# Kernel tuning notes

Hardware: AMD Instinct MI355X
Metric: run time of the kernel (lower is better)

## Reference

```python
import jax, jax.numpy as jnp
import numpy as np

N = 50000   # nodes
E = 500000  # edges
S = 64      # 0e channels in node feats
V = 32      # 1o channels in node feats
R = 32      # radial/scalar edge features
MLPW = 128
AVG = 10.0  # avg_num_neighbors
SQ3 = np.float32(np.sqrt(3.0))
SQ2 = np.float32(np.sqrt(2.0))


def setup_inputs() -> dict:
    key = jax.random.key(0)
    ks = jax.random.split(key, 10)
    node_scalars = jax.random.normal(ks[0], (N, S), jnp.float32)
    node_vectors = jax.random.normal(ks[1], (N, V, 3), jnp.float32)
    ev = jax.random.normal(ks[2], (E, 3), jnp.float32)
    # l=1 spherical harmonics of unit edge vectors, component normalization (|Y1| = sqrt(3))
    edge_vec = ev / jnp.linalg.norm(ev, axis=1, keepdims=True) * SQ3
    scalar_edge_feats = jax.random.normal(ks[3], (E, R), jnp.float32)
    lengths = jax.random.uniform(ks[4], (E, 1), jnp.float32)
    senders = jax.random.randint(ks[5], (E,), 0, N, jnp.int32)
    receivers = jax.random.randint(ks[6], (E,), 0, N, jnp.int32)
    din = 2 * S + R + 1  # 161
    num_irreps = V + (S + V)  # 128 gate scalars
    def lin(k, i, o):
        return jax.random.normal(k, (i, o), jnp.float32) / np.float32(np.sqrt(i))
    return {
        "node_scalars": node_scalars, "node_vectors": node_vectors,
        "edge_vec": edge_vec, "scalar_edge_feats": scalar_edge_feats,
        "lengths": lengths, "senders": senders, "receivers": receivers,
        "W1": lin(ks[7], din, MLPW), "b1": jnp.zeros((MLPW,), jnp.float32),
        "W2": lin(ks[8], MLPW, MLPW), "b2": jnp.zeros((MLPW,), jnp.float32),
        "W3": lin(ks[9], MLPW, num_irreps), "b3": jnp.zeros((num_irreps,), jnp.float32),
    }


def reference(node_scalars, node_vectors, edge_vec, scalar_edge_feats, lengths,
              senders, receivers, W1, b1, W2, b2, W3, b3):
    # gather sender features
    s_snd = node_scalars[senders]          # [E, S]
    v_snd = node_vectors[senders]          # [E, V, 3]
    # Clebsch-Gordan tensor product with 1o edge harmonics (component normalization):
    m0 = jnp.einsum('eca,ea->ec', v_snd, edge_vec) / SQ3          # 1o x 1o -> 0e, [E, V]
    m1a = s_snd[:, :, None] * edge_vec[:, None, :]                 # 0e x 1o -> 1o, [E, S, 3]
    m1b = jnp.cross(v_snd, edge_vec[:, None, :]) / SQ2             # 1o x 1o -> 1o, [E, V, 3]
    # MLP gate on concatenated scalars
    mlp_in = jnp.concatenate([s_snd, node_scalars[receivers], scalar_edge_feats, lengths], axis=1)
    h = jax.nn.silu(mlp_in @ W1 + b1)
    h = jax.nn.silu(h @ W2 + b2)
    mix = h @ W3 + b3                                               # [E, V + S + V]
    m0 = m0 * mix[:, :V]
    m1 = jnp.concatenate([m1a, m1b], axis=1) * mix[:, V:, None]     # [E, S+V, 3]
    # scatter-add to receivers
    out0 = jax.ops.segment_sum(m0, receivers, num_segments=N)      # [N, V]
    out1 = jax.ops.segment_sum(m1, receivers, num_segments=N)      # [N, S+V, 3]
    return jnp.concatenate([out0, out1.reshape(N, -1)], axis=1) / AVG
```

## Files before the change

### kernel.cpp

```cpp
#include <hip/hip_runtime.h>

#define N_NODES 50000
#define N_EDGES 500000
#define EB 64
#define AST 184
#define HST 136
#define W1K 176
#define OUTC 320
#define MROW 208
#define NBLK1 49
#define KP1 200
#define KH  136
#define KV  104
#define WTS 40
#define INV_SQ3 0.57735026918962576f
#define INV_SQ2 0.70710678118654752f
#define INV_AVG 0.1f

typedef short bf16x8 __attribute__((ext_vector_type(8)));
typedef unsigned short u16;
typedef u16 u16x8 __attribute__((ext_vector_type(8)));
typedef float f32x16 __attribute__((ext_vector_type(16)));

template <int N> struct IC { static constexpr int val = N; };

__device__ __forceinline__ unsigned cvtpk(float lo, float hi) {
    unsigned r;
    asm("v_cvt_pk_bf16_f32 %0, %1, %2" : "=v"(r) : "v"(lo), "v"(hi));
    return r;
}
__device__ __forceinline__ u16 f2bf(float f) { return (u16)cvtpk(f, f); }
__device__ __forceinline__ float bf2f(u16 h) {
    union { unsigned u; float f; } x; x.u = ((unsigned)h) << 16; return x.f;
}
__device__ __forceinline__ float fsilu(float x) {
    return x * __builtin_amdgcn_rcpf(1.f + __expf(-x));
}

__device__ __forceinline__ void stage16(const float* g, u16* l, bool v) {
    float4 a0, a1, a2, a3;
    const float4 z = make_float4(0.f, 0.f, 0.f, 0.f);
    if (v) { a0 = *(const float4*)(g);     a1 = *(const float4*)(g + 4);
             a2 = *(const float4*)(g + 8); a3 = *(const float4*)(g + 12); }
    else   { a0 = z; a1 = z; a2 = z; a3 = z; }
    uint4 p0 = { cvtpk(a0.x, a0.y), cvtpk(a0.z, a0.w), cvtpk(a1.x, a1.y), cvtpk(a1.z, a1.w) };
    uint4 p1 = { cvtpk(a2.x, a2.y), cvtpk(a2.z, a2.w), cvtpk(a3.x, a3.y), cvtpk(a3.z, a3.w) };
    *(uint4*)(l) = p0; *(uint4*)(l + 8) = p1;
}
__device__ __forceinline__ void stage8(const float* g, u16* l, bool v) {
    float4 a0, a1;
    const float4 z = make_float4(0.f, 0.f, 0.f, 0.f);
    if (v) { a0 = *(const float4*)(g); a1 = *(const float4*)(g + 4); }
    else   { a0 = z; a1 = z; }
    uint4 p0 = { cvtpk(a0.x, a0.y), cvtpk(a0.z, a0.w), cvtpk(a1.x, a1.y), cvtpk(a1.z, a1.w) };
    *(uint4*)(l) = p0;
}


__global__ void hist_kernel(const int* __restrict__ recv, int* __restrict__ counts) {
    const int e = blockIdx.x * 256 + threadIdx.x;
    if (e < N_EDGES) atomicAdd(&counts[recv[e]], 1);
}

__global__ __launch_bounds__(256) void scan_k1(const int* __restrict__ counts,
                                               int* __restrict__ rowp,
                                               int* __restrict__ partials) {
    __shared__ int sd[256];
    const int t = threadIdx.x;
    const int base = blockIdx.x * 1024 + t * 4;
    int c0 = 0, c1 = 0, c2 = 0, c3 = 0;
    if (base + 3 < N_NODES) {
        int4 v = *(const int4*)&counts[base];
        c0 = v.x; c1 = v.y; c2 = v.z; c3 = v.w;
    } else {
        if (base     < N_NODES) c0 = counts[base];
        if (base + 1 < N_NODES) c1 = counts[base + 1];
        if (base + 2 < N_NODES) c2 = counts[base + 2];
        if (base + 3 < N_NODES) c3 = counts[base + 3];
    }
    const int T = c0 + c1 + c2 + c3;
    sd[t] = T; __syncthreads();
    for (int off = 1; off < 256; off <<= 1) {
        int v = (t >= off) ? sd[t - off] : 0;
        __syncthreads();
        sd[t] += v;
        __syncthreads();
    }
    const int excl = sd[t] - T;
    if (base     < N_NODES) rowp[base]     = excl;
    if (base + 1 < N_NODES) rowp[base + 1] = excl + c0;
    if (base + 2 < N_NODES) rowp[base + 2] = excl + c0 + c1;
    if (base + 3 < N_NODES) rowp[base + 3] = excl + c0 + c1 + c2;
    if (t == 255) partials[blockIdx.x] = sd[255];
}

__global__ __launch_bounds__(64) void scan_k2(int* __restrict__ partials) {
    __shared__ int sd[64];
    const int t = threadIdx.x;
    const int v0 = (t < NBLK1) ? partials[t] : 0;
    sd[t] = v0; __syncthreads();
    for (int off = 1; off < 64; off <<= 1) {
        int v = (t >= off) ? sd[t - off] : 0;
        __syncthreads();
        sd[t] += v;
        __syncthreads();
    }
    if (t < NBLK1) partials[t] = sd[t] - v0;
}

__global__ __launch_bounds__(256) void scan_k3(int* __restrict__ rowp,
                                               const int* __restrict__ partials,
                                               int* __restrict__ cursors) {
    const int add = partials[blockIdx.x];
    const int base = blockIdx.x * 1024 + threadIdx.x * 4;
    #pragma unroll
    for (int i = 0; i < 4; ++i) {
        const int idx = base + i;
        if (idx < N_NODES) {
            const int v = rowp[idx] + add;
            rowp[idx] = v;
            cursors[idx] = v;
        }
    }
    if (blockIdx.x == 0 && threadIdx.x == 0) rowp[N_NODES] = N_EDGES;
}

__global__ void fill_kernel(const int* __restrict__ recv,
                            int* __restrict__ cursors, int* __restrict__ elist) {
    const int e = blockIdx.x * 256 + threadIdx.x;
    if (e < N_EDGES) {
        const int r = recv[e];
        const int pos = atomicAdd(&cursors[r], 1);
        elist[pos] = e;
    }
}


#define WT_TOTAL (128 * W1K + 2 * 128 * 128)

__global__ __launch_bounds__(256)
void wcvt_kernel(const float* __restrict__ W1, const float* __restrict__ W2,
                 const float* __restrict__ W3, u16* __restrict__ wt) {
    const int i = blockIdx.x * 256 + threadIdx.x;
    if (i < 128 * W1K) {
        const int n = i / W1K, k = i - n * W1K;
        wt[i] = (k < 161) ? f2bf(W1[(size_t)k * 128 + n]) : (u16)0;
    } else if (i < 128 * W1K + 128 * 128) {
        const int j = i - 128 * W1K;
        const int n = j >> 7, k = j & 127;
        wt[i] = f2bf(W2[(size_t)k * 128 + n]);
    } else if (i < WT_TOTAL) {
        const int j = i - 128 * W1K - 128 * 128;
        const int n = j >> 7, k = j & 127;
        wt[i] = f2bf(W3[(size_t)k * 128 + n]);
    }
}


#define NS_ELEMS (N_NODES * 64)
#define NV_ELEMS (N_NODES * 96)

__global__ __launch_bounds__(256)
void nodecvt_kernel(const float* __restrict__ ns, const float* __restrict__ nv,
                    u16* __restrict__ nsb, u16* __restrict__ nvb) {
    const int i2 = (blockIdx.x * 256 + threadIdx.x) * 2;
    if (i2 < NS_ELEMS) {
        float2 v = *(const float2*)(ns + i2);
        *(unsigned*)(nsb + i2) = cvtpk(v.x, v.y);
    } else if (i2 < NS_ELEMS + NV_ELEMS) {
        const int j2 = i2 - NS_ELEMS;
        float2 v = *(const float2*)(nv + j2);
        *(unsigned*)(nvb + j2) = cvtpk(v.x, v.y);
    }
}


__global__ __launch_bounds__(256, 4)
void mlp_msg_kernel(const u16* __restrict__ ns_bf,
                    const u16* __restrict__ nv_bf,
                    const float* __restrict__ edge_vec,
                    const float* __restrict__ sef,
                    const float* __restrict__ lengths,
                    const int* __restrict__ senders,
                    const int* __restrict__ receivers,
                    const int* __restrict__ elist,
                    const u16* __restrict__ wt,
                    const float* __restrict__ b1,
                    const float* __restrict__ b2,
                    const float* __restrict__ b3,
                    u16* __restrict__ msg, int slo, int cnt)
{
    __shared__ u16 A [EB * AST];
    __shared__ u16 Hb[EB * HST];

    const int t = threadIdx.x;
    const int lbase = blockIdx.x * EB;
    const int me = t >> 2, q = t & 3;
    const int ls = lbase + me;
    const bool ve = ls < cnt;
    const int eid = ve ? elist[slo + ls] : 0;

    {   const int si = senders[eid];
        const int ri = receivers[eid];
        u16* Ar = A + me * AST;
        const u16* srow = ns_bf + (size_t)si * 64 + q * 16;
        const u16* rrow = ns_bf + (size_t)ri * 64 + q * 16;
        *(u16x8*)(Ar + q * 16)          = *(const u16x8*)(srow);
        *(u16x8*)(Ar + q * 16 + 8)      = *(const u16x8*)(srow + 8);
        *(u16x8*)(Ar + 64 + q * 16)     = *(const u16x8*)(rrow);
        *(u16x8*)(Ar + 64 + q * 16 + 8) = *(const u16x8*)(rrow + 8);
        stage8(sef + (size_t)eid * 32 + q * 8, Ar + 128 + q * 8, true);
        if (q == 0) {
            u16x8 z8 = (u16x8)0;
            z8[0] = f2bf(lengths[eid]);
            *(u16x8*)(Ar + 160) = z8;
            const float evx = edge_vec[(size_t)eid * 3 + 0];
            const float evy = edge_vec[(size_t)eid * 3 + 1];
            const float evz = edge_vec[(size_t)eid * 3 + 2];
            const unsigned bx = __builtin_bit_cast(unsigned, evx);
            const unsigned by = __builtin_bit_cast(unsigned, evy);
            const unsigned bz = __builtin_bit_cast(unsigned, evz);
            u16x8 p;
            p[0] = (u16)(bx & 0xFFFF); p[1] = (u16)(bx >> 16);
            p[2] = (u16)(by & 0xFFFF); p[3] = (u16)(by >> 16);
            p[4] = (u16)(bz & 0xFFFF); p[5] = (u16)(bz >> 16);
            p[6] = (u16)si;            p[7] = 0;
            *(u16x8*)(Hb + me * HST + 128) = p;
        } else if (q == 1) {
            *(u16x8*)(A + me * AST + 168) = (u16x8)0;
        }
    }
    __syncthreads();

    const int w  = t >> 6, l = t & 63;
    const int lr = l & 31;
    const int lg = l >> 5;
    const int m0 = (w >> 1) * 32;
    const int n0 = (w & 1) * 64;

    const u16* w1t = wt;
    const u16* w2t = wt + 128 * W1K;
    const u16* w3t = w2t + 128 * 128;

    f32x16 acc0, acc1;

    auto run_layer = [&](const u16* Asrc, int astr, const u16* Wg, int wstr, auto NS,
                         f32x16& a0, f32x16& a1) {
        #pragma unroll
        for (int i = 0; i < 16; ++i) { a0[i] = 0.f; a1[i] = 0.f; }
        const u16* ap  = Asrc + (m0 + lr) * astr + lg * 8;
        const u16* bp0 = Wg + (size_t)(n0 + lr) * wstr + lg * 8;
        const u16* bp1 = bp0 + 32 * wstr;
        #pragma unroll
        for (int ks = 0; ks < NS.val; ++ks) {
            bf16x8 af  = *(const bf16x8*)(ap  + ks * 16);
            bf16x8 bv0 = *(const bf16x8*)(bp0 + ks * 16);
            bf16x8 bv1 = *(const bf16x8*)(bp1 + ks * 16);
            a0 = __builtin_amdgcn_mfma_f32_32x32x16_bf16(af, bv0, a0, 0, 0, 0);
            a1 = __builtin_amdgcn_mfma_f32_32x32x16_bf16(af, bv1, a1, 0, 0, 0);
        }
    };

    run_layer(A, AST, w1t, W1K, IC<11>{}, acc0, acc1);
    __syncthreads();
    {   const float bv0 = b1[n0 + lr], bv1 = b1[n0 + 32 + lr];
        #pragma unroll
        for (int r = 0; r < 16; ++r) {
            const int row = (r & 3) + 8 * (r >> 2) + 4 * lg;
            Hb[(m0 + row) * HST + n0 + lr]      = f2bf(fsilu(acc0[r] + bv0));
            Hb[(m0 + row) * HST + n0 + 32 + lr] = f2bf(fsilu(acc1[r] + bv1));
        }
    }
    {
        const int si2 = (int)Hb[me * HST + 134];
        const u16* src = nv_bf + (size_t)si2 * 96 + q * 24;
        u16* dst = A + me * AST + 64 + q * 24;
        *(u16x8*)(dst)      = *(const u16x8*)(src);
        *(u16x8*)(dst + 8)  = *(const u16x8*)(src + 8);
        *(u16x8*)(dst + 16) = *(const u16x8*)(src + 16);
    }
    __syncthreads();

    run_layer(Hb, HST, w2t, 128, IC<8>{}, acc0, acc1);
    __syncthreads();
    {   const float bv0 = b2[n0 + lr], bv1 = b2[n0 + 32 + lr];
        #pragma unroll
        for (int r = 0; r < 16; ++r) {
            const int row = (r & 3) + 8 * (r >> 2) + 4 * lg;
            Hb[(m0 + row) * HST + n0 + lr]      = f2bf(fsilu(acc0[r] + bv0));
            Hb[(m0 + row) * HST + n0 + 32 + lr] = f2bf(fsilu(acc1[r] + bv1));
        }
    }
    __syncthreads();

    run_layer(Hb, HST, w3t, 128, IC<8>{}, acc0, acc1);
    __syncthreads();
    {   const float bv0 = b3[n0 + lr], bv1 = b3[n0 + 32 + lr];
        #pragma unroll
        for (int r = 0; r < 16; ++r) {
            const int row = (r & 3) + 8 * (r >> 2) + 4 * lg;
            Hb[(m0 + row) * HST + n0 + lr]      = f2bf(acc0[r] + bv0);
            Hb[(m0 + row) * HST + n0 + 32 + lr] = f2bf(acc1[r] + bv1);
        }
    }
    __syncthreads();

    if (ve) {
        const u16* Ar = A  + me * AST;
        const u16* Vr = Ar + 64;
        const u16* Hr = Hb + me * HST;
        const u16* Er = Hr + 128;
        u16* mrow = msg + (size_t)ls * MROW;
        const float evx = __builtin_bit_cast(float, (unsigned)Er[0] | ((unsigned)Er[1] << 16));
        const float evy = __builtin_bit_cast(float, (unsigned)Er[2] | ((unsigned)Er[3] << 16));
        const float evz = __builtin_bit_cast(float, (unsigned)Er[4] | ((unsigned)Er[5] << 16));

        float m0v[8], m1bv[24];
        #pragma unroll
        for (int j = 0; j < 8; ++j) {
            const int c = 8 * q + j;
            const float vx = bf2f(Vr[3 * c]), vy = bf2f(Vr[3 * c + 1]), vz = bf2f(Vr[3 * c + 2]);
            m0v[j] = (vx * evx + vy * evy + vz * evz) * INV_SQ3 * bf2f(Hr[c]);
            const float gb = bf2f(Hr[96 + c]) * INV_SQ2;
            m1bv[3 * j + 0] = (vy * evz - vz * evy) * gb;
            m1bv[3 * j + 1] = (vz * evx - vx * evz) * gb;
            m1bv[3 * j + 2] = (vx * evy - vy * evx) * gb;
        }
        {   uint4 o = { cvtpk(m0v[0], m0v[1]), cvtpk(m0v[2], m0v[3]),
                        cvtpk(m0v[4], m0v[5]), cvtpk(m0v[6], m0v[7]) };
            *(uint4*)(mrow + 8 * q) = o;
        }
        {   u16* dst = mrow + 96 + 24 * q;
            uint4 o0 = { cvtpk(m1bv[0],  m1bv[1]),  cvtpk(m1bv[2],  m1bv[3]),
                         cvtpk(m1bv[4],  m1bv[5]),  cvtpk(m1bv[6],  m1bv[7])  };
            uint4 o1 = { cvtpk(m1bv[8],  m1bv[9]),  cvtpk(m1bv[10], m1bv[11]),
                         cvtpk(m1bv[12], m1bv[13]), cvtpk(m1bv[14], m1bv[15]) };
            uint4 o2 = { cvtpk(m1bv[16], m1bv[17]), cvtpk(m1bv[18], m1bv[19]),
                         cvtpk(m1bv[20], m1bv[21]), cvtpk(m1bv[22], m1bv[23]) };
            *(uint4*)(dst)      = o0;
            *(uint4*)(dst + 8)  = o1;
            *(uint4*)(dst + 16) = o2;
        }
        {   float sg[16];
            #pragma unroll
            for (int j = 0; j < 16; ++j) {
                const int k = 16 * q + j;
                sg[j] = bf2f(Ar[k]) * bf2f(Hr[32 + k]);
            }
            u16* dst = mrow + 32 + 16 * q;
            uint4 o0 = { cvtpk(sg[0],  sg[1]),  cvtpk(sg[2],  sg[3]),
                         cvtpk(sg[4],  sg[5]),  cvtpk(sg[6],  sg[7])  };
            uint4 o1 = { cvtpk(sg[8],  sg[9]),  cvtpk(sg[10], sg[11]),
                         cvtpk(sg[12], sg[13]), cvtpk(sg[14], sg[15]) };
            *(uint4*)(dst)     = o0;
            *(uint4*)(dst + 8) = o1;
        }
        if (q == 0) {
            uint4 e4 = { __builtin_bit_cast(unsigned, evx),
                         __builtin_bit_cast(unsigned, evy),
                         __builtin_bit_cast(unsigned, evz), 0u };
            *(uint4*)(mrow + 192) = e4;
            uint4 z4 = { 0u, 0u, 0u, 0u };
            *(uint4*)(mrow + 200) = z4;
        }
    }
}


__global__ __launch_bounds__(256)
void msg_gather_seq(const int* __restrict__ rowp,
                    const u16* __restrict__ msg,
                    float* __restrict__ out,
                    int slo, int shi, int first)
{
    __shared__ float oacc[4][OUTC];

    const int gw = (blockIdx.x * 256 + threadIdx.x) >> 6;
    const int l  = threadIdx.x & 63;
    const bool nvalid = gw < N_NODES;

    const int rp0 = nvalid ? rowp[gw] : 0;
    const int rp1 = nvalid ? rowp[gw + 1] : 0;
    const int lo = rp0 > slo ? rp0 : slo;
    const int hi = rp1 < shi ? rp1 : shi;
    const int n  = hi > lo ? hi - lo : 0;

    const int half = (l >= 26) ? 1 : 0;
    const int sl   = l - 26 * half;
    const bool lact = (l < 52) && (sl < 24);
    const int seg  = (sl < 4) ? 0 : (sl < 12 ? 1 : 2);

    float acc[24];
    #pragma unroll
    for (int i = 0; i < 24; ++i) acc[i] = 0.f;

    const u16* mb = msg + (size_t)(lo - slo) * MROW;

    auto body = [&](int row) {
        const u16* rp = mb + (size_t)row * MROW + sl * 8;
        const u16x8 v = *(const u16x8*)rp;
        if (seg == 1) {
            const float4 e4 = *(const float4*)(mb + (size_t)row * MROW + 192);
            #pragma unroll
            for (int i = 0; i < 8; ++i) {
                const float s = bf2f(v[i]);
                acc[3 * i + 0] += s * e4.x;
                acc[3 * i + 1] += s * e4.y;
                acc[3 * i + 2] += s * e4.z;
            }
        } else {
            #pragma unroll
            for (int i = 0; i < 8; ++i) acc[i] += bf2f(v[i]);
        }
    };

    int j = 0;
    for (; j + 2 <= n; j += 2) {
        if (lact) body(j + half);
    }
    if (j < n && half == 0 && lact) body(j);

    float* oa = oacc[(threadIdx.x >> 6)];

    if (half == 0 && lact) {
        if (seg == 0) {
            #pragma unroll
            for (int i = 0; i < 8; ++i) oa[sl * 8 + i] = acc[i];
        } else if (seg == 1) {
            const int k0 = (sl - 4) * 8;
            #pragma unroll
            for (int i = 0; i < 8; ++i) {
                oa[32 + 3 * (k0 + i) + 0] = acc[3 * i + 0];
                oa[32 + 3 * (k0 + i) + 1] = acc[3 * i + 1];
                oa[32 + 3 * (k0 + i) + 2] = acc[3 * i + 2];
            }
        } else {
            const int c0 = (sl - 12) * 8;
            #pragma unroll
            for (int i = 0; i < 8; ++i) oa[224 + c0 + i] = acc[i];
        }
    }
    __syncthreads();
    if (half == 1 && lact) {
        if (seg == 0) {
            #pragma unroll
            for (int i = 0; i < 8; ++i) oa[sl * 8 + i] += acc[i];
        } else if (seg == 1) {
            const int k0 = (sl - 4) * 8;
            #pragma unroll
            for (int i = 0; i < 8; ++i) {
                oa[32 + 3 * (k0 + i) + 0] += acc[3 * i + 0];
                oa[32 + 3 * (k0 + i) + 1] += acc[3 * i + 1];
                oa[32 + 3 * (k0 + i) + 2] += acc[3 * i + 2];
            }
        } else {
            const int c0 = (sl - 12) * 8;
            #pragma unroll
            for (int i = 0; i < 8; ++i) oa[224 + c0 + i] += acc[i];
        }
    }
    __syncthreads();

    if (nvalid && l < 40) {
        float r[8];
        #pragma unroll
        for (int i = 0; i < 8; ++i) r[i] = oa[l * 8 + i] * INV_AVG;
        float* orow = out + (size_t)gw * OUTC + l * 8;
        if (first) {
            *(float4*)(orow)     = make_float4(r[0], r[1], r[2], r[3]);
            *(float4*)(orow + 4) = make_float4(r[4], r[5], r[6], r[7]);
        } else if (n > 0) {
            float4 p0 = *(const float4*)(orow);
            float4 p1 = *(const float4*)(orow + 4);
            p0.x += r[0]; p0.y += r[1]; p0.z += r[2]; p0.w += r[3];
            p1.x += r[4]; p1.y += r[5]; p1.z += r[6]; p1.w += r[7];
            *(float4*)(orow)     = p0;
            *(float4*)(orow + 4) = p1;
        }
    }
}


__global__ __launch_bounds__(256, 2)
void fused_mpconv_atomic(const float* __restrict__ node_scalars,
                         const float* __restrict__ node_vectors,
                         const float* __restrict__ edge_vec,
                         const float* __restrict__ sef,
                         const float* __restrict__ lengths,
                         const int* __restrict__ senders,
                         const int* __restrict__ receivers,
                         const float* __restrict__ W1, const float* __restrict__ b1,
                         const float* __restrict__ W2, const float* __restrict__ b2,
                         const float* __restrict__ W3, const float* __restrict__ b3,
                         float* __restrict__ out)
{
    __shared__ u16 A [EB * KP1];
    __shared__ u16 VS[EB * KV];
    __shared__ u16 Hb[EB * KH];
    __shared__ u16 Wt[2][128 * WTS];
    __shared__ float evl[3][EB];
    __shared__ int sidx[EB], ridx[EB];

    const int t = threadIdx.x;
    const int ebase = blockIdx.x * EB;

    {   const int e = t & 63, sub = t >> 6;
        const int eg = ebase + e; const bool ve = eg < N_EDGES;
        if (sub == 0)      sidx[e] = ve ? senders[eg] : 0;
        else if (sub == 1) ridx[e] = ve ? receivers[eg] : 0;
        else if (sub == 2) {
            evl[0][e] = ve ? edge_vec[(size_t)eg * 3 + 0] : 0.f;
            evl[1][e] = ve ? edge_vec[(size_t)eg * 3 + 1] : 0.f;
            evl[2][e] = ve ? edge_vec[(size_t)eg * 3 + 2] : 0.f;
        }
    }
    __syncthreads();

    {   const int me = t >> 2, q = t & 3;
        const int eg = ebase + me; const bool ve = eg < N_EDGES;
        const int si = sidx[me], ri = ridx[me];
        u16* Ar = A + me * KP1;
        stage16(node_scalars + (size_t)si * 64 + q * 16, Ar + q * 16,       ve);
        stage16(node_scalars + (size_t)ri * 64 + q * 16, Ar + 64 + q * 16,  ve);
        stage8 (sef          + (size_t)eg * 32 + q * 8,  Ar + 128 + q * 8,  ve);
        u16x8 zz = (u16x8)0;
        *(u16x8*)(Ar + 160 + q * 8) = zz;
        if (q == 0) *(u16x8*)(Ar + 192) = zz;
        stage16(node_vectors + (size_t)si * 96 + q * 24,      VS + me * KV + q * 24,      ve);
        stage8 (node_vectors + (size_t)si * 96 + q * 24 + 16, VS + me * KV + q * 24 + 16, ve);
        if (q == 0) Ar[160] = f2bf(ve ? lengths[eg] : 0.f);
    }
    __syncthreads();

    const int w  = t >> 6, l = t & 63;
    const int lr = l & 31;
    const int lg = l >> 5;
    const int m0 = (w >> 1) * 32;
    const int n0 = (w & 1) * 64;

    f32x16 acc0, acc1;
    const int n  = t & 127, ph = t >> 7;

    auto run_layer = [&](const u16* Asrc, int astr, const float* Wg, int Kr, int nsteps,
                         f32x16& a0, f32x16& a1) {
        #pragma unroll
        for (int i = 0; i < 16; ++i) { a0[i] = 0.f; a1[i] = 0.f; }
        #pragma unroll
        for (int i = 0; i < 4; ++i) {
            int kl = (i * 2 + ph) * 2;
            float v0 = (kl     < Kr) ? Wg[(size_t)kl * 128 + n]       : 0.f;
            float v1 = (kl + 1 < Kr) ? Wg[(size_t)(kl + 1) * 128 + n] : 0.f;
            *(unsigned*)&Wt[0][n * WTS + kl] = cvtpk(v0, v1);
        }
        __syncthreads();
        const u16* ap = Asrc + (m0 + lr) * astr + lg * 8;
        for (int ks = 0; ks < nsteps; ++ks) {
            const int cur = ks & 1;
            float v0[4], v1[4];
            const int kb = (ks + 1) * 16;
            if (ks + 1 < nsteps) {
                #pragma unroll
                for (int i = 0; i < 4; ++i) {
                    int kg = kb + (i * 2 + ph) * 2;
                    v0[i] = (kg     < Kr) ? Wg[(size_t)kg * 128 + n]       : 0.f;
                    v1[i] = (kg + 1 < Kr) ? Wg[(size_t)(kg + 1) * 128 + n] : 0.f;
                }
            }
            bf16x8 af = *(const bf16x8*)(ap + ks * 16);
            bf16x8 bf0 = *(const bf16x8*)(&Wt[cur][(n0      + lr) * WTS + lg * 8]);
            bf16x8 bf1 = *(const bf16x8*)(&Wt[cur][(n0 + 32 + lr) * WTS + lg * 8]);
            a0 = __builtin_amdgcn_mfma_f32_32x32x16_bf16(af, bf0, a0, 0, 0, 0);
            a1 = __builtin_amdgcn_mfma_f32_32x32x16_bf16(af, bf1, a1, 0, 0, 0);
            if (ks + 1 < nsteps) {
                #pragma unroll
                for (int i = 0; i < 4; ++i) {
                    int kl = (i * 2 + ph) * 2;
                    *(unsigned*)&Wt[cur ^ 1][n * WTS + kl] = cvtpk(v0[i], v1[i]);
                }
            }
            __syncthreads();
        }
    };

    run_layer(A, KP1, W1, 161, 11, acc0, acc1);
    {   const float bv0 = b1[n0 + lr], bv1 = b1[n0 + 32 + lr];
        #pragma unroll
        for (int r = 0; r < 16; ++r) {
            const int row = (r & 3) + 8 * (r >> 2) + 4 * lg;
            Hb[(m0 + row) * KH + n0 + lr]      = f2bf(fsilu(acc0[r] + bv0));
            Hb[(m0 + row) * KH + n0 + 32 + lr] = f2bf(fsilu(acc1[r] + bv1));
        }
    }
    __syncthreads();

    run_layer(Hb, KH, W2, 128, 8, acc0, acc1);
    __syncthreads();
    {   const float bv0 = b2[n0 + lr], bv1 = b2[n0 + 32 + lr];
        #pragma unroll
        for (int r = 0; r < 16; ++r) {
            const int row = (r & 3) + 8 * (r >> 2) + 4 * lg;
            Hb[(m0 + row) * KH + n0 + lr]      = f2bf(fsilu(acc0[r] + bv0));
            Hb[(m0 + row) * KH + n0 + 32 + lr] = f2bf(fsilu(acc1[r] + bv1));
        }
    }
    __syncthreads();

    run_layer(Hb, KH, W3, 128, 8, acc0, acc1);
    __syncthreads();
    {   const float bv0 = b3[n0 + lr], bv1 = b3[n0 + 32 + lr];
        #pragma unroll
        for (int r = 0; r < 16; ++r) {
            const int row = (r & 3) + 8 * (r >> 2) + 4 * lg;
            Hb[(m0 + row) * KH + n0 + lr]      = f2bf(acc0[r] + bv0);
            Hb[(m0 + row) * KH + n0 + 32 + lr] = f2bf(acc1[r] + bv1);
        }
    }
    __syncthreads();

    {   const int me = t >> 2, r = t & 3;
        const int eg2 = ebase + me;
        if (eg2 < N_EDGES) {
            const int row = ridx[me];
            const float evx = evl[0][me], evy = evl[1][me], evz = evl[2][me];
            float* orow = out + (size_t)row * OUTC;
            const u16* Ar = A  + me * KP1;
            const u16* Vr = VS + me * KV;
            const u16* Hr = Hb + me * KH;
            for (int col = r; col < OUTC; col += 4) {
                float val;
                if (col < 32) {
                    const int c = col;
                    const float vx = bf2f(Vr[3 * c]), vy = bf2f(Vr[3 * c + 1]), vz = bf2f(Vr[3 * c + 2]);
                    val = (vx * evx + vy * evy + vz * evz) * INV_SQ3 * bf2f(Hr[c]);
                } else {
                    const int idx = col - 32;
                    const int k = idx / 3;
                    const int d = idx - 3 * k;
                    const float g = bf2f(Hr[32 + k]);
                    if (k < 64) {
                        const float evd = (d == 0) ? evx : ((d == 1) ? evy : evz);
                        val = bf2f(Ar[k]) * evd * g;
                    } else {
                        const int c = k - 64;
                        const float vx = bf2f(Vr[3 * c]), vy = bf2f(Vr[3 * c + 1]), vz = bf2f(Vr[3 * c + 2]);
                        float cr;
                        if (d == 0)      cr = vy * evz - vz * evy;
                        else if (d == 1) cr = vz * evx - vx * evz;
                        else             cr = vx * evy - vy * evx;
                        val = cr * INV_SQ2 * g;
                    }
                }
                atomicAdd(&orow[col], val * INV_AVG);
            }
        }
    }
}


extern "C" void kernel_launch(void* const* d_in, const int* in_sizes, int n_in,
                              void* d_out, int out_size, void* d_ws, size_t ws_size,
                              hipStream_t stream) {
    (void)in_sizes; (void)n_in;
    const float* node_scalars = (const float*)d_in[0];
    const float* node_vectors = (const float*)d_in[1];
    const float* edge_vec     = (const float*)d_in[2];
    const float* sef          = (const float*)d_in[3];
    const float* lengths      = (const float*)d_in[4];
    const int*   senders      = (const int*)d_in[5];
    const int*   receivers    = (const int*)d_in[6];
    const float* W1 = (const float*)d_in[7];
    const float* b1 = (const float*)d_in[8];
    const float* W2 = (const float*)d_in[9];
    const float* b2 = (const float*)d_in[10];
    const float* W3 = (const float*)d_in[11];
    const float* b3 = (const float*)d_in[12];
    float* out = (float*)d_out;

    auto align256 = [](size_t x) { return (x + 255) & ~(size_t)255; };

    size_t off = 0;
    const size_t o_counts  = off; off += align256((size_t)N_NODES * sizeof(int));
    const size_t o_rowp    = off; off += align256((size_t)(N_NODES + 1) * sizeof(int));
    const size_t o_cursors = off; off += align256((size_t)(N_NODES + 1) * sizeof(int));
    const size_t o_part    = off; off += align256(64 * sizeof(int));
    const size_t o_elist   = off; off += align256((size_t)N_EDGES * sizeof(int));
    const size_t o_wt      = off; off += align256((size_t)WT_TOTAL * sizeof(u16));
    const size_t o_nsb     = off; off += align256((size_t)NS_ELEMS * sizeof(u16));
    const size_t o_nvb     = off; off += align256((size_t)NV_ELEMS * sizeof(u16));
    const size_t o_msg     = off;
    const size_t fixed_bytes = off;

    const size_t ROWB = (size_t)MROW * sizeof(u16);
    long Ec = 0;
    if (ws_size > fixed_bytes + (size_t)128 * ROWB) {
        size_t cap_rows = (ws_size - fixed_bytes) / ROWB;
        Ec = ((long)cap_rows - 64) / 64 * 64;
        if (Ec > N_EDGES) Ec = N_EDGES;
    }

    char* ws = (char*)d_ws;

    if (Ec >= 64) {
        int* counts  = (int*)(ws + o_counts);
        int* rowp    = (int*)(ws + o_rowp);
        int* cursors = (int*)(ws + o_cursors);
        int* part    = (int*)(ws + o_part);
        int* elist   = (int*)(ws + o_elist);
        u16* wt      = (u16*)(ws + o_wt);
        u16* nsb     = (u16*)(ws + o_nsb);
        u16* nvb     = (u16*)(ws + o_nvb);
        u16* msg     = (u16*)(ws + o_msg);

        hipMemsetAsync(counts, 0, (size_t)N_NODES * sizeof(int), stream);
        hist_kernel<<<(N_EDGES + 255) / 256, 256, 0, stream>>>(receivers, counts);
        scan_k1<<<NBLK1, 256, 0, stream>>>(counts, rowp, part);
        scan_k2<<<1, 64, 0, stream>>>(part);
        scan_k3<<<NBLK1, 256, 0, stream>>>(rowp, part, cursors);
        fill_kernel<<<(N_EDGES + 255) / 256, 256, 0, stream>>>(receivers, cursors, elist);
        wcvt_kernel<<<(WT_TOTAL + 255) / 256, 256, 0, stream>>>(W1, W2, W3, wt);
        nodecvt_kernel<<<((NS_ELEMS + NV_ELEMS) / 2 + 255) / 256, 256, 0, stream>>>(
            node_scalars, node_vectors, nsb, nvb);

        const int nchunks = (int)((N_EDGES + Ec - 1) / Ec);
        const int ggrid = (N_NODES * 64 + 255) / 256;
        for (int c = 0; c < nchunks; ++c) {
            const int slo = (int)(c * Ec);
            const int cnt = (int)((N_EDGES - slo < Ec) ? (N_EDGES - slo) : Ec);
            mlp_msg_kernel<<<(cnt + EB - 1) / EB, 256, 0, stream>>>(
                nsb, nvb, edge_vec, sef, lengths, senders, receivers,
                elist, wt, b1, b2, b3, msg, slo, cnt);
            msg_gather_seq<<<ggrid, 256, 0, stream>>>(
                rowp, msg, out, slo, slo + cnt, c == 0 ? 1 : 0);
        }
    } else {
        hipMemsetAsync(out, 0, (size_t)out_size * sizeof(float), stream);
        fused_mpconv_atomic<<<(N_EDGES + EB - 1) / EB, 256, 0, stream>>>(
            node_scalars, node_vectors, edge_vec, sef, lengths,
            senders, receivers, W1, b1, W2, b2, W3, b3, out);
    }
}
```

Measured before the change: 375.6 us.

## Pre-permute edge data into receiver order and load MLP inputs directly into registers

Adds an edge permutation kernel that writes the per-edge features, lengths and edge vectors into receiver-sorted slot order, and has the fill kernel emit permuted sender and receiver arrays. The MLP kernel then loads the first-layer A fragments straight from global memory into registers, removing the LDS A tile and one barrier stage, and occupancy is raised to 5 blocks per SM. Vector features are now read directly per edge in the epilogue. The gather loop is also unrolled by two. This trades an extra pass over the edge data plus more workspace for coalesced reads and less LDS in the main kernel.

Result: slower. 461.7 us (+22.9%).

```diff
diff --git a/kernel.cpp b/kernel.cpp
--- a/kernel.cpp
+++ b/kernel.cpp
@@ -3,7 +3,6 @@
 #define N_NODES 50000
 #define N_EDGES 500000
 #define EB 64
-#define AST 184
 #define HST 136
 #define W1K 176
 #define OUTC 320
@@ -21,8 +20,6 @@
 typedef unsigned short u16;
 typedef u16 u16x8 __attribute__((ext_vector_type(8)));
 typedef float f32x16 __attribute__((ext_vector_type(16)));
-
-template <int N> struct IC { static constexpr int val = N; };
 
 __device__ __forceinline__ unsigned cvtpk(float lo, float hi) {
     unsigned r;
@@ -126,12 +123,18 @@
 }
 
 __global__ void fill_kernel(const int* __restrict__ recv,
-                            int* __restrict__ cursors, int* __restrict__ elist) {
+                            const int* __restrict__ snd,
+                            int* __restrict__ cursors,
+                            int* __restrict__ elist,
+                            int* __restrict__ esnd,
+                            int* __restrict__ ercv) {
     const int e = blockIdx.x * 256 + threadIdx.x;
     if (e < N_EDGES) {
         const int r = recv[e];
         const int pos = atomicAdd(&cursors[r], 1);
         elist[pos] = e;
+        esnd[pos]  = snd[e];
+        ercv[pos]  = r;
     }
 }
 
@@ -175,68 +178,85 @@
 }
 
 
-__global__ __launch_bounds__(256, 4)
+__global__ __launch_bounds__(256)
+void edgeperm_kernel(const int* __restrict__ elist,
+                     const float* __restrict__ sef,
+                     const float* __restrict__ len,
+                     const float* __restrict__ ev,
+                     u16* __restrict__ sefp,
+                     u16* __restrict__ lenp,
+                     float* __restrict__ evp) {
+    const int s2 = blockIdx.x * 256 + threadIdx.x;
+    const int slot = s2 >> 1, h = s2 & 1;
+    if (slot >= N_EDGES) return;
+    const int e = elist[slot];
+    const float* src = sef + (size_t)e * 32 + h * 16;
+    u16* dst = sefp + (size_t)slot * 32 + h * 16;
+    float4 a0 = ((const float4*)src)[0], a1 = ((const float4*)src)[1];
+    float4 a2 = ((const float4*)src)[2], a3 = ((const float4*)src)[3];
+    uint4 p0 = { cvtpk(a0.x, a0.y), cvtpk(a0.z, a0.w), cvtpk(a1.x, a1.y), cvtpk(a1.z, a1.w) };
+    uint4 p1 = { cvtpk(a2.x, a2.y), cvtpk(a2.z, a2.w), cvtpk(a3.x, a3.y), cvtpk(a3.z, a3.w) };
+    ((uint4*)dst)[0] = p0; ((uint4*)dst)[1] = p1;
+    if (h == 0) {
+        lenp[slot] = f2bf(len[e]);
+        const float* ep = ev + (size_t)e * 3;
+        float* dp = evp + (size_t)slot * 3;
+        dp[0] = ep[0]; dp[1] = ep[1]; dp[2] = ep[2];
+    }
+}
+
+
+__global__ __launch_bounds__(256, 5)
 void mlp_msg_kernel(const u16* __restrict__ ns_bf,
                     const u16* __restrict__ nv_bf,
-                    const float* __restrict__ edge_vec,
-                    const float* __restrict__ sef,
-                    const float* __restrict__ lengths,
-                    const int* __restrict__ senders,
-                    const int* __restrict__ receivers,
-                    const int* __restrict__ elist,
+                    const int* __restrict__ esnd,
+                    const int* __restrict__ ercv,
+                    const u16* __restrict__ sefp,
+                    const u16* __restrict__ lenp,
+                    const float* __restrict__ evp,
                     const u16* __restrict__ wt,
                     const float* __restrict__ b1,
                     const float* __restrict__ b2,
                     const float* __restrict__ b3,
                     u16* __restrict__ msg, int slo, int cnt)
 {
-    __shared__ u16 A [EB * AST];
     __shared__ u16 Hb[EB * HST];
 
     const int t = threadIdx.x;
     const int lbase = blockIdx.x * EB;
+    const int w = t >> 6, l = t & 63;
+    const int lr = l & 31, lg = l >> 5;
+    const int m0 = (w >> 1) * 32, n0 = (w & 1) * 64;
+
+    const int lsA   = lbase + m0 + lr;
+    const int slotA = slo + (lsA < cnt ? lsA : 0);
+    const int siA = esnd[slotA];
+    const int riA = ercv[slotA];
+
     const int me = t >> 2, q = t & 3;
-    const int ls = lbase + me;
-    const bool ve = ls < cnt;
-    const int eid = ve ? elist[slo + ls] : 0;
-
-    {   const int si = senders[eid];
-        const int ri = receivers[eid];
-        u16* Ar = A + me * AST;
-        const u16* srow = ns_bf + (size_t)si * 64 + q * 16;
-        const u16* rrow = ns_bf + (size_t)ri * 64 + q * 16;
-        *(u16x8*)(Ar + q * 16)          = *(const u16x8*)(srow);
-        *(u16x8*)(Ar + q * 16 + 8)      = *(const u16x8*)(srow + 8);
-        *(u16x8*)(Ar + 64 + q * 16)     = *(const u16x8*)(rrow);
-        *(u16x8*)(Ar + 64 + q * 16 + 8) = *(const u16x8*)(rrow + 8);
-        stage8(sef + (size_t)eid * 32 + q * 8, Ar + 128 + q * 8, true);
-        if (q == 0) {
-            u16x8 z8 = (u16x8)0;
-            z8[0] = f2bf(lengths[eid]);
-            *(u16x8*)(Ar + 160) = z8;
-            const float evx = edge_vec[(size_t)eid * 3 + 0];
-            const float evy = edge_vec[(size_t)eid * 3 + 1];
-            const float evz = edge_vec[(size_t)eid * 3 + 2];
-            const unsigned bx = __builtin_bit_cast(unsigned, evx);
-            const unsigned by = __builtin_bit_cast(unsigned, evy);
-            const unsigned bz = __builtin_bit_cast(unsigned, evz);
-            u16x8 p;
-            p[0] = (u16)(bx & 0xFFFF); p[1] = (u16)(bx >> 16);
-            p[2] = (u16)(by & 0xFFFF); p[3] = (u16)(by >> 16);
-            p[4] = (u16)(bz & 0xFFFF); p[5] = (u16)(bz >> 16);
-            p[6] = (u16)si;            p[7] = 0;
-            *(u16x8*)(Hb + me * HST + 128) = p;
-        } else if (q == 1) {
-            *(u16x8*)(A + me * AST + 168) = (u16x8)0;
-        }
-    }
-    __syncthreads();
-
-    const int w  = t >> 6, l = t & 63;
-    const int lr = l & 31;
-    const int lg = l >> 5;
-    const int m0 = (w >> 1) * 32;
-    const int n0 = (w & 1) * 64;
+    const int lsE = lbase + me;
+    const bool veE = lsE < cnt;
+    const int slotE = slo + (veE ? lsE : 0);
+    const int siE = esnd[slotE];
+    const float evx = evp[(size_t)slotE * 3 + 0];
+    const float evy = evp[(size_t)slotE * 3 + 1];
+    const float evz = evp[(size_t)slotE * 3 + 2];
+
+    bf16x8 afr[11];
+    {
+        const u16* sp = ns_bf + (size_t)siA * 64 + lg * 8;
+        const u16* rp = ns_bf + (size_t)riA * 64 + lg * 8;
+        const u16* fp = sefp + (size_t)slotA * 32 + lg * 8;
+        #pragma unroll
+        for (int ks = 0; ks < 4; ++ks) afr[ks]     = *(const bf16x8*)(sp + ks * 16);
+        #pragma unroll
+        for (int ks = 0; ks < 4; ++ks) afr[4 + ks] = *(const bf16x8*)(rp + ks * 16);
+        afr[8] = *(const bf16x8*)(fp);
+        afr[9] = *(const bf16x8*)(fp + 16);
+        bf16x8 z = (bf16x8)0;
+        if (lg == 0) z[0] = (short)lenp[slotA];
+        afr[10] = z;
+    }
 
     const u16* w1t = wt;
     const u16* w2t = wt + 128 * W1K;
@@ -244,15 +264,37 @@
 
     f32x16 acc0, acc1;
 
-    auto run_layer = [&](const u16* Asrc, int astr, const u16* Wg, int wstr, auto NS,
-                         f32x16& a0, f32x16& a1) {
+    #pragma unroll
+    for (int i = 0; i < 16; ++i) { acc0[i] = 0.f; acc1[i] = 0.f; }
+    {
+        const u16* bp0 = w1t + (size_t)(n0 + lr) * W1K + lg * 8;
+        const u16* bp1 = bp0 + 32 * W1K;
+        #pragma unroll
+        for (int ks = 0; ks < 11; ++ks) {
+            bf16x8 bv0 = *(const bf16x8*)(bp0 + ks * 16);
+            bf16x8 bv1 = *(const bf16x8*)(bp1 + ks * 16);
+            acc0 = __builtin_amdgcn_mfma_f32_32x32x16_bf16(afr[ks], bv0, acc0, 0, 0, 0);
+            acc1 = __builtin_amdgcn_mfma_f32_32x32x16_bf16(afr[ks], bv1, acc1, 0, 0, 0);
+        }
+    }
+    {   const float bv0 = b1[n0 + lr], bv1 = b1[n0 + 32 + lr];
+        #pragma unroll
+        for (int r = 0; r < 16; ++r) {
+            const int row = (r & 3) + 8 * (r >> 2) + 4 * lg;
+            Hb[(m0 + row) * HST + n0 + lr]      = f2bf(fsilu(acc0[r] + bv0));
+            Hb[(m0 + row) * HST + n0 + 32 + lr] = f2bf(fsilu(acc1[r] + bv1));
+        }
+    }
+    __syncthreads();
+
+    auto run_layer_lds = [&](const u16* Wg, f32x16& a0, f32x16& a1) {
         #pragma unroll
         for (int i = 0; i < 16; ++i) { a0[i] = 0.f; a1[i] = 0.f; }
-        const u16* ap  = Asrc + (m0 + lr) * astr + lg * 8;
-        const u16* bp0 = Wg + (size_t)(n0 + lr) * wstr + lg * 8;
-        const u16* bp1 = bp0 + 32 * wstr;
-        #pragma unroll
-        for (int ks = 0; ks < NS.val; ++ks) {
+        const u16* ap  = Hb + (m0 + lr) * HST + lg * 8;
+        const u16* bp0 = Wg + (size_t)(n0 + lr) * 128 + lg * 8;
+        const u16* bp1 = bp0 + 32 * 128;
+        #pragma unroll
+        for (int ks = 0; ks < 8; ++ks) {
             bf16x8 af  = *(const bf16x8*)(ap  + ks * 16);
             bf16x8 bv0 = *(const bf16x8*)(bp0 + ks * 16);
             bf16x8 bv1 = *(const bf16x8*)(bp1 + ks * 16);
@@ -261,9 +303,9 @@
         }
     };
 
-    run_layer(A, AST, w1t, W1K, IC<11>{}, acc0, acc1);
-    __syncthreads();
-    {   const float bv0 = b1[n0 + lr], bv1 = b1[n0 + 32 + lr];
+    run_layer_lds(w2t, acc0, acc1);
+    __syncthreads();
+    {   const float bv0 = b2[n0 + lr], bv1 = b2[n0 + 32 + lr];
         #pragma unroll
         for (int r = 0; r < 16; ++r) {
             const int row = (r & 3) + 8 * (r >> 2) + 4 * lg;
@@ -271,29 +313,9 @@
             Hb[(m0 + row) * HST + n0 + 32 + lr] = f2bf(fsilu(acc1[r] + bv1));
         }
     }
-    {
-        const int si2 = (int)Hb[me * HST + 134];
-        const u16* src = nv_bf + (size_t)si2 * 96 + q * 24;
-        u16* dst = A + me * AST + 64 + q * 24;
-        *(u16x8*)(dst)      = *(const u16x8*)(src);
-        *(u16x8*)(dst + 8)  = *(const u16x8*)(src + 8);
-        *(u16x8*)(dst + 16) = *(const u16x8*)(src + 16);
-    }
-    __syncthreads();
-
-    run_layer(Hb, HST, w2t, 128, IC<8>{}, acc0, acc1);
-    __syncthreads();
-    {   const float bv0 = b2[n0 + lr], bv1 = b2[n0 + 32 + lr];
-        #pragma unroll
-        for (int r = 0; r < 16; ++r) {
-            const int row = (r & 3) + 8 * (r >> 2) + 4 * lg;
-            Hb[(m0 + row) * HST + n0 + lr]      = f2bf(fsilu(acc0[r] + bv0));
-            Hb[(m0 + row) * HST + n0 + 32 + lr] = f2bf(fsilu(acc1[r] + bv1));
-        }
-    }
-    __syncthreads();
-
-    run_layer(Hb, HST, w3t, 128, IC<8>{}, acc0, acc1);
+    __syncthreads();
+
+    run_layer_lds(w3t, acc0, acc1);
     __syncthreads();
     {   const float bv0 = b3[n0 + lr], bv1 = b3[n0 + 32 + lr];
         #pragma unroll
@@ -305,21 +327,26 @@
     }
     __syncthreads();
 
-    if (ve) {
-        const u16* Ar = A  + me * AST;
-        const u16* Vr = Ar + 64;
+    if (veE) {
         const u16* Hr = Hb + me * HST;
-        const u16* Er = Hr + 128;
-        u16* mrow = msg + (size_t)ls * MROW;
-        const float evx = __builtin_bit_cast(float, (unsigned)Er[0] | ((unsigned)Er[1] << 16));
-        const float evy = __builtin_bit_cast(float, (unsigned)Er[2] | ((unsigned)Er[3] << 16));
-        const float evz = __builtin_bit_cast(float, (unsigned)Er[4] | ((unsigned)Er[5] << 16));
+        u16* mrow = msg + (size_t)lsE * MROW;
+
+        u16 sa[16], va[24];
+        {
+            const u16* nsrow = ns_bf + (size_t)siE * 64 + 16 * q;
+            *(u16x8*)(sa)     = *(const u16x8*)(nsrow);
+            *(u16x8*)(sa + 8) = *(const u16x8*)(nsrow + 8);
+            const u16* nvrow = nv_bf + (size_t)siE * 96 + 24 * q;
+            *(u16x8*)(va)      = *(const u16x8*)(nvrow);
+            *(u16x8*)(va + 8)  = *(const u16x8*)(nvrow + 8);
+            *(u16x8*)(va + 16) = *(const u16x8*)(nvrow + 16);
+        }
 
         float m0v[8], m1bv[24];
         #pragma unroll
         for (int j = 0; j < 8; ++j) {
             const int c = 8 * q + j;
-            const float vx = bf2f(Vr[3 * c]), vy = bf2f(Vr[3 * c + 1]), vz = bf2f(Vr[3 * c + 2]);
+            const float vx = bf2f(va[3 * j]), vy = bf2f(va[3 * j + 1]), vz = bf2f(va[3 * j + 2]);
             m0v[j] = (vx * evx + vy * evy + vz * evz) * INV_SQ3 * bf2f(Hr[c]);
             const float gb = bf2f(Hr[96 + c]) * INV_SQ2;
             m1bv[3 * j + 0] = (vy * evz - vz * evy) * gb;
@@ -345,7 +372,7 @@
             #pragma unroll
             for (int j = 0; j < 16; ++j) {
                 const int k = 16 * q + j;
-                sg[j] = bf2f(Ar[k]) * bf2f(Hr[32 + k]);
+                sg[j] = bf2f(sa[j]) * bf2f(Hr[32 + k]);
             }
             u16* dst = mrow + 32 + 16 * q;
             uint4 o0 = { cvtpk(sg[0],  sg[1]),  cvtpk(sg[2],  sg[3]),
@@ -415,6 +442,9 @@
     };
 
     int j = 0;
+    for (; j + 4 <= n; j += 4) {
+        if (lact) { body(j + half); body(j + 2 + half); }
+    }
     for (; j + 2 <= n; j += 2) {
         if (lact) body(j + half);
     }
@@ -684,9 +714,14 @@
     const size_t o_cursors = off; off += align256((size_t)(N_NODES + 1) * sizeof(int));
     const size_t o_part    = off; off += align256(64 * sizeof(int));
     const size_t o_elist   = off; off += align256((size_t)N_EDGES * sizeof(int));
+    const size_t o_esnd    = off; off += align256((size_t)N_EDGES * sizeof(int));
+    const size_t o_ercv    = off; off += align256((size_t)N_EDGES * sizeof(int));
     const size_t o_wt      = off; off += align256((size_t)WT_TOTAL * sizeof(u16));
     const size_t o_nsb     = off; off += align256((size_t)NS_ELEMS * sizeof(u16));
     const size_t o_nvb     = off; off += align256((size_t)NV_ELEMS * sizeof(u16));
+    const size_t o_sefp    = off; off += align256((size_t)N_EDGES * 32 * sizeof(u16));
+    const size_t o_lenp    = off; off += align256((size_t)N_EDGES * sizeof(u16));
+    const size_t o_evp     = off; off += align256((size_t)N_EDGES * 3 * sizeof(float));
     const size_t o_msg     = off;
     const size_t fixed_bytes = off;
 
@@ -706,9 +741,14 @@
         int* cursors = (int*)(ws + o_cursors);
         int* part    = (int*)(ws + o_part);
         int* elist   = (int*)(ws + o_elist);
+        int* esnd    = (int*)(ws + o_esnd);
+        int* ercv    = (int*)(ws + o_ercv);
         u16* wt      = (u16*)(ws + o_wt);
         u16* nsb     = (u16*)(ws + o_nsb);
         u16* nvb     = (u16*)(ws + o_nvb);
+        u16* sefp    = (u16*)(ws + o_sefp);
+        u16* lenp    = (u16*)(ws + o_lenp);
+        float* evp   = (float*)(ws + o_evp);
         u16* msg     = (u16*)(ws + o_msg);
 
         hipMemsetAsync(counts, 0, (size_t)N_NODES * sizeof(int), stream);
@@ -716,7 +756,10 @@
         scan_k1<<<NBLK1, 256, 0, stream>>>(counts, rowp, part);
         scan_k2<<<1, 64, 0, stream>>>(part);
         scan_k3<<<NBLK1, 256, 0, stream>>>(rowp, part, cursors);
-        fill_kernel<<<(N_EDGES + 255) / 256, 256, 0, stream>>>(receivers, cursors, elist);
+        fill_kernel<<<(N_EDGES + 255) / 256, 256, 0, stream>>>(
+            receivers, senders, cursors, elist, esnd, ercv);
+        edgeperm_kernel<<<(N_EDGES * 2 + 255) / 256, 256, 0, stream>>>(
+            elist, sef, lengths, edge_vec, sefp, lenp, evp);
         wcvt_kernel<<<(WT_TOTAL + 255) / 256, 256, 0, stream>>>(W1, W2, W3, wt);
         nodecvt_kernel<<<((NS_ELEMS + NV_ELEMS) / 2 + 255) / 256, 256, 0, stream>>>(
             node_scalars, node_vectors, nsb, nvb);
@@ -727,8 +770,8 @@
             const int slo = (int)(c * Ec);
             const int cnt = (int)((N_EDGES - slo < Ec) ? (N_EDGES - slo) : Ec);
             mlp_msg_kernel<<<(cnt + EB - 1) / EB, 256, 0, stream>>>(
-                nsb, nvb, edge_vec, sef, lengths, senders, receivers,
-                elist, wt, b1, b2, b3, msg, slo, cnt);
+                nsb, nvb, esnd, ercv, sefp, lenp, evp,
+                wt, b1, b2, b3, msg, slo, cnt);
             msg_gather_seq<<<ggrid, 256, 0, stream>>>(
                 rowp, msg, out, slo, slo + cnt, c == 0 ? 1 : 0);
         }
```
